# Performance work log

Measured on AMD Instinct MI355X. Metric: run time of the kernel, lower is better.

## Reference

```python
import jax, jax.numpy as jnp
import numpy as np


def conv(x, w, groups=1):
    # x: NCHW, w: OIHW, stride 1, SAME padding
    return jax.lax.conv_general_dilated(
        x, w, (1, 1), 'SAME', feature_group_count=groups,
        dimension_numbers=('NCHW', 'OIHW', 'NCHW'))


def bn(x, scale, shift):
    # eval-mode BatchNorm folded into per-channel affine
    return x * scale[None, :, None, None] + shift[None, :, None, None]


def ghost_expert(x, Wp, sp, bp, Wc, sc, bc, out_ch):
    # primary conv 3x3 (C_in -> init_ch) + BN + SiLU
    x1 = jax.nn.silu(bn(conv(x, Wp), sp, bp))
    # cheap depthwise 3x3 (groups = init_ch) + BN + SiLU
    x2 = jax.nn.silu(bn(conv(x1, Wc, groups=x1.shape[1]), sc, bc))
    return jnp.concatenate([x1, x2], axis=1)[:, :out_ch]


def setup_inputs() -> dict:
    key = jax.random.key(0)
    ks = jax.random.split(key, 20)
    B, Cin, Cout, H, W = 8, 256, 256, 64, 64
    E, red, init_ch, new_ch = 4, 32, 128, 128
    f = lambda k, shape, s=0.05: jax.random.normal(k, shape, jnp.float32) * s
    g = lambda k, shape: jax.random.uniform(k, shape, jnp.float32, 0.5, 1.5)
    inp = dict(
        x=jax.random.normal(ks[0], (B, Cin, H, W), jnp.float32),
        # router: conv3x3 Cin->red, BN, SiLU, conv1x1 red->E, BN
        Wr1=f(ks[1], (red, Cin, 3, 3)), sr1=g(ks[2], (red,)), br1=f(ks[3], (red,), 0.1),
        Wr2=f(ks[4], (E, red, 1, 1)), sr2=g(ks[5], (E,)), br2=f(ks[6], (E,), 0.1),
        # E ghost experts (stacked on leading expert axis)
        We_p=f(ks[7], (E, init_ch, Cin, 3, 3)), se_p=g(ks[8], (E, init_ch)), be_p=f(ks[9], (E, init_ch), 0.1),
        We_c=f(ks[10], (E, new_ch, 1, 3, 3)), se_c=g(ks[11], (E, new_ch)), be_c=f(ks[12], (E, new_ch), 0.1),
        # shared ghost expert
        Ws_p=f(ks[13], (init_ch, Cin, 3, 3)), ss_p=g(ks[14], (init_ch,)), bs_p=f(ks[15], (init_ch,), 0.1),
        Ws_c=f(ks[16], (new_ch, 1, 3, 3)), ss_c=g(ks[17], (new_ch,)), bs_c=f(ks[18], (new_ch,), 0.1),
        top_k=2,
    )
    return inp


def reference(x, Wr1, sr1, br1, Wr2, sr2, br2,
              We_p, se_p, be_p, We_c, se_c, be_c,
              Ws_p, ss_p, bs_p, Ws_c, ss_c, bs_c, top_k):
    B, Cin, H, W = x.shape
    E = Wr2.shape[0]
    Cout = 256
    pool_scale = 4
    # ---- EfficientSpatialRouter (eval mode: no noise) ----
    xd = x.reshape(B, Cin, H // pool_scale, pool_scale, W // pool_scale, pool_scale).mean((3, 5))
    h = jax.nn.silu(bn(conv(xd, Wr1), sr1, br1))
    logits = bn(conv(h, Wr2), sr2, br2)           # [B, E, H/4, W/4]
    global_logits = logits.mean(axis=(2, 3))      # [B, E]
    weights = jax.nn.softmax(global_logits, axis=1)
    topk_vals, topk_idx = jax.lax.top_k(weights, top_k)
    topk_vals = topk_vals / (topk_vals.sum(axis=1, keepdims=True) + 1e-6)
    # ---- dense all-expert compute + weighted combine ----
    run = lambda Wp, sp, bp, Wc, sc, bc: ghost_expert(x, Wp, sp, bp, Wc, sc, bc, Cout)
    expert_outs = jax.vmap(run)(We_p, se_p, be_p, We_c, se_c, be_c)  # [E,B,Cout,H,W]
    w_full = (topk_vals[:, :, None] * jax.nn.one_hot(topk_idx, E, dtype=x.dtype)).sum(1)  # [B,E]
    combined = jnp.einsum('be,ebchw->bchw', w_full, expert_outs)
    # ---- shared expert for stability ----
    shared = ghost_expert(x, Ws_p, ss_p, bs_p, Ws_c, ss_c, bs_c, Cout)
    return combined + shared
```

## Files before the change

kernel.cpp:

```cpp
#include <hip/hip_runtime.h>
#include <hip/hip_bf16.h>

constexpr int BATCH = 8;
constexpr int CIN   = 256;
constexpr int HH    = 64;
constexpr int WW    = 64;
constexpr int NPIX  = HH * WW;
constexpr int ICH   = 128;

constexpr size_t OFF_XD    = 0;
constexpr size_t OFF_HMEAN = 524288;
constexpr size_t OFF_WFULL = 524544;
constexpr size_t OFF_SLOT  = 524608;
constexpr size_t OFF_WTB   = 524672;
constexpr size_t OFF_XB    = OFF_WTB + 737280;
constexpr size_t OFF_X1B   = OFF_XB + 4194304;

typedef __bf16  bf16x8 __attribute__((ext_vector_type(8)));
typedef float   f32x4  __attribute__((ext_vector_type(4)));

__device__ __forceinline__ float silu_f(float v) { return v / (1.f + __expf(-v)); }

__device__ __forceinline__ unsigned short f2bf(float f) {
    return __builtin_bit_cast(unsigned short, __float2bfloat16(f));
}
__device__ __forceinline__ float bf2f(unsigned short u) {
    return __builtin_bit_cast(float, (unsigned)u << 16);
}
__device__ __forceinline__ bf16x8 ld_frag(const ushort* p) {
    uint4 v = *(const uint4*)p;
    return __builtin_bit_cast(bf16x8, v);
}

__global__ void k_avgpool(const float* __restrict__ x, float* __restrict__ xd)
{
    int t = blockIdx.x * 256 + threadIdx.x;
    int jb = t & 3, i = (t >> 2) & 15, c = (t >> 6) & 255, b = t >> 14;
    const float* src = x + ((size_t)(b * CIN + c) * HH + i * 4) * WW + jb * 16;
    float s0 = 0.f, s1 = 0.f, s2 = 0.f, s3 = 0.f;
#pragma unroll
    for (int r = 0; r < 4; ++r) {
        const float4* p = (const float4*)(src + r * WW);
        float4 a = p[0], b4 = p[1], c4 = p[2], d4 = p[3];
        s0 += a.x + a.y + a.z + a.w;
        s1 += b4.x + b4.y + b4.z + b4.w;
        s2 += c4.x + c4.y + c4.z + c4.w;
        s3 += d4.x + d4.y + d4.z + d4.w;
    }
    float4 o;
    o.x = s0 * 0.0625f; o.y = s1 * 0.0625f; o.z = s2 * 0.0625f; o.w = s3 * 0.0625f;
    *(float4*)(xd + ((size_t)(b * CIN + c) * 16 + i) * 16 + jb * 4) = o;
}

__global__ __launch_bounds__(256) void k_xprep(const float* __restrict__ x,
                                               ushort* __restrict__ xb)
{
    int b = blockIdx.x >> 6, row = blockIdx.x & 63;
    __shared__ ushort tile[64 * 258];
    int tid = threadIdx.x;
    const float* src = x + ((size_t)b * CIN * HH + row) * WW;
    for (int k = tid; k < 256 * 64; k += 256) {
        int cin = k >> 6, col = k & 63;
        tile[col * 258 + cin] = f2bf(src[(size_t)cin * NPIX + col]);
    }
    __syncthreads();
    ushort* dst = xb + (size_t)(b * 64 + row) * 64 * 256;
    for (int k = tid; k < 64 * 128; k += 256) {
        int col = k >> 7, cp = (k & 127) * 2;
        unsigned u0 = tile[col * 258 + cp];
        unsigned u1 = tile[col * 258 + cp + 1];
        *(unsigned*)(dst + (size_t)col * 256 + cp) = u0 | (u1 << 16);
    }
}

__global__ __launch_bounds__(256) void k_router_conv(
    const float* __restrict__ xd, const float* __restrict__ Wr1,
    const float* __restrict__ sr1, const float* __restrict__ br1,
    float* __restrict__ hmean)
{
    int b = blockIdx.x >> 5, r = blockIdx.x & 31;
    __shared__ float wl[9 * 256];
    __shared__ float red[256];
    int tid = threadIdx.x;
    for (int k = tid; k < 2304; k += 256) {
        int cin = k / 9, tap = k % 9;
        wl[tap * 256 + cin] = Wr1[r * 2304 + k];
    }
    __syncthreads();
    const float* xb = xd + (size_t)b * CIN * 256;
    int i = tid >> 4, j = tid & 15;
    float acc = 0.f;
#pragma unroll
    for (int kh = 0; kh < 3; ++kh) {
        int ii = i + kh - 1;
        bool oki = (unsigned)ii < 16u;
        int iis = oki ? ii : 0;
#pragma unroll
        for (int kw = 0; kw < 3; ++kw) {
            int jj = j + kw - 1;
            bool ok = oki && ((unsigned)jj < 16u);
            int off = iis * 16 + (((unsigned)jj < 16u) ? jj : 0);
            const float* wt = wl + (kh * 3 + kw) * 256;
            float t = 0.f;
#pragma unroll 8
            for (int cin = 0; cin < 256; ++cin)
                t = fmaf(wt[cin], xb[cin * 256 + off], t);
            if (ok) acc += t;
        }
    }
    float h = silu_f(acc * sr1[r] + br1[r]);
    red[tid] = h;
    __syncthreads();
    for (int st = 128; st > 0; st >>= 1) {
        if (tid < st) red[tid] += red[tid + st];
        __syncthreads();
    }
    if (tid == 0) hmean[b * 32 + r] = red[0] * (1.f / 256.f);
}

__global__ void k_router_final(const float* __restrict__ hmean,
                               const float* __restrict__ Wr2, const float* __restrict__ sr2,
                               const float* __restrict__ br2, const int* __restrict__ topk_p,
                               float* __restrict__ wfull, int* __restrict__ slot)
{
    __shared__ float lg[8][4];
    __shared__ float wf[8][5];
    int tid = threadIdx.x;
    if (tid < 32) {
        int b = tid >> 2, e = tid & 3;
        float a = 0.f;
        for (int r = 0; r < 32; ++r) a += Wr2[e * 32 + r] * hmean[b * 32 + r];
        lg[b][e] = a * sr2[e] + br2[e];
    }
    __syncthreads();
    if (tid < 8) {
        int b = tid;
        float l0 = lg[b][0], l1 = lg[b][1], l2 = lg[b][2], l3 = lg[b][3];
        float mx = fmaxf(fmaxf(l0, l1), fmaxf(l2, l3));
        float e0 = __expf(l0 - mx), e1 = __expf(l1 - mx), e2 = __expf(l2 - mx), e3 = __expf(l3 - mx);
        float sum = e0 + e1 + e2 + e3;
        float w[4] = { e0 / sum, e1 / sum, e2 / sum, e3 / sum };
        int k = topk_p[0];
        if (k > 4) k = 4;
        bool taken[4] = { false, false, false, false };
        float tv[4]; int ti[4]; float tsum = 0.f;
        for (int t = 0; t < k; ++t) {
            float best = -1e30f; int bi = 0;
            for (int e = 0; e < 4; ++e)
                if (!taken[e] && w[e] > best) { best = w[e]; bi = e; }
            taken[bi] = true; tv[t] = best; ti[t] = bi; tsum += best;
        }
        float inv = 1.f / (tsum + 1e-6f);
        float o[4] = { 0.f, 0.f, 0.f, 0.f };
        for (int t = 0; t < k; ++t) o[ti[t]] = tv[t] * inv;
        for (int e = 0; e < 4; ++e) { wf[b][e] = o[e]; wfull[b * 5 + e] = o[e]; }
        wf[b][4] = 1.f; wfull[b * 5 + 4] = 1.f;
    }
    __syncthreads();
    if (tid == 0) {
        int cnt = 0;
        for (int s = 0; s < 5; ++s)
            for (int b = 0; b < 8; ++b)
                slot[s * 8 + b] = (wf[b][s] != 0.f) ? (cnt++) : -1;
    }
}

__global__ void k_wprep16(const float* __restrict__ We_p, const float* __restrict__ Ws_p,
                          ushort* __restrict__ wtb)
{
    int t = blockIdx.x * 256 + threadIdx.x;
    int k5  = t & 31;
    int oc  = (t >> 5) & 63;
    int tap = (t >> 11) % 9;
    int blk = t / 18432;
    int chunk = blk & 7;
    int h     = (blk >> 3) & 1;
    int s     = blk >> 4;
    int cin   = chunk * 32 + k5;
    int ocg   = h * 64 + oc;
    float v = (s < 4) ? We_p[((size_t)(s * 128 + ocg) * 256 + cin) * 9 + tap]
                      : Ws_p[((size_t)ocg * 256 + cin) * 9 + tap];
    wtb[t] = f2bf(v);
}

__global__ __launch_bounds__(256, 2) void k_primary_mfma(
    const ushort* __restrict__ xb, const ushort* __restrict__ wtb,
    const float* __restrict__ se_p, const float* __restrict__ be_p,
    const float* __restrict__ ss_p, const float* __restrict__ bs_p,
    const int* __restrict__ slot, ushort* __restrict__ x1b)
{
    int pass = blockIdx.y;
    int sl = slot[pass];
    if (sl < 0) return;
    int s = pass >> 3, b = pass & 7;
    int och = blockIdx.x >> 4;
    int tile = blockIdx.x & 15;
    int row0 = (tile >> 2) * 16, col0 = (tile & 3) * 16;

    __shared__ ushort wlds[2304 * 8];
    __shared__ ushort xlds[1296 * 8];

    int tid = threadIdx.x;
    int w = tid >> 6, l = tid & 63;
    int ks = l >> 4, c = l & 15;

    f32x4 acc[4][4];
#pragma unroll
    for (int m = 0; m < 4; ++m)
#pragma unroll
        for (int n = 0; n < 4; ++n) acc[m][n] = (f32x4){0.f, 0.f, 0.f, 0.f};

    const ushort* wslab = wtb + (size_t)(s * 2 + och) * 8 * 18432;
    const ushort* xbase = xb + (size_t)b * 64 * 64 * 256;

    for (int ch = 0; ch < 8; ++ch) {
        __syncthreads();
        const ushort* wsrc = wslab + ch * 18432;
        for (int k = tid; k < 2304; k += 256) {
            uint4 v = *(const uint4*)(wsrc + k * 8);
            *(uint4*)(wlds + k * 8) = v;
        }
        int cin0 = ch * 32;
        for (int k = tid; k < 1296; k += 256) {
            int r = k / 72, rem = k % 72;
            int ks2 = rem / 18, c2 = rem % 18;
            int gr = row0 + r - 1, gc = col0 + c2 - 1;
            uint4 v = make_uint4(0u, 0u, 0u, 0u);
            if ((unsigned)gr < 64u && (unsigned)gc < 64u)
                v = *(const uint4*)(xbase + ((size_t)gr * 64 + gc) * 256 + cin0 + ks2 * 8);
            *(uint4*)(xlds + (size_t)k * 8) = v;
        }
        __syncthreads();
#pragma unroll
        for (int kh = 0; kh < 3; ++kh) {
#pragma unroll
            for (int kw = 0; kw < 3; ++kw) {
                int tap = kh * 3 + kw;
                bf16x8 afr[4];
#pragma unroll
                for (int m = 0; m < 4; ++m)
                    afr[m] = ld_frag(wlds + ((size_t)(tap * 64 + m * 16 + c) * 4 + ks) * 8);
#pragma unroll
                for (int n = 0; n < 4; ++n) {
                    int rloc = 4 * w + n + kh;
                    bf16x8 bfr = ld_frag(xlds + ((size_t)(rloc * 4 + ks) * 18 + c + kw) * 8);
#pragma unroll
                    for (int m = 0; m < 4; ++m)
                        acc[m][n] = __builtin_amdgcn_mfma_f32_16x16x32_bf16(
                            afr[m], bfr, acc[m][n], 0, 0, 0);
                }
            }
        }
    }

    const float* scale = (s < 4) ? (se_p + s * ICH) : ss_p;
    const float* shift = (s < 4) ? (be_p + s * ICH) : bs_p;
    ushort* outp = x1b + (size_t)sl * (ICH * NPIX);
    int colg = col0 + c;
#pragma unroll
    for (int m = 0; m < 4; ++m) {
#pragma unroll
        for (int n = 0; n < 4; ++n) {
            int rowg = row0 + 4 * w + n;
#pragma unroll
            for (int j = 0; j < 4; ++j) {
                int oc = och * 64 + m * 16 + ks * 4 + j;
                float v = acc[m][n][j] * scale[oc] + shift[oc];
                outp[(size_t)oc * NPIX + rowg * 64 + colg] = f2bf(silu_f(v));
            }
        }
    }
}

__global__ __launch_bounds__(256) void k_cheap(
    const ushort* __restrict__ x1b, const float* __restrict__ We_c,
    const float* __restrict__ se_c, const float* __restrict__ be_c,
    const float* __restrict__ Ws_c, const float* __restrict__ ss_c,
    const float* __restrict__ bs_c, const float* __restrict__ wfull,
    const int* __restrict__ slot, float* __restrict__ out)
{
    int blk = blockIdx.x;
    int b = blk >> 7, c = blk & 127;
    __shared__ float img[66][66];
    int tid = threadIdx.x;
    for (int k = tid; k < 66 * 66; k += 256) ((float*)img)[k] = 0.f;
    float o1[16], o2[16];
#pragma unroll
    for (int t = 0; t < 16; ++t) { o1[t] = 0.f; o2[t] = 0.f; }
    __syncthreads();

    for (int s = 0; s < 5; ++s) {
        int sl = slot[s * 8 + b];
        if (sl < 0) continue;
        float wgt = (s < 4) ? wfull[b * 5 + s] : 1.0f;
        const ushort* src = x1b + ((size_t)sl * ICH + c) * NPIX;
        for (int k = tid; k < NPIX / 2; k += 256) {
            int i = k >> 5, jc = (k & 31) * 2;
            unsigned u = *(const unsigned*)(src + i * 64 + jc);
            img[1 + i][1 + jc] = bf2f((unsigned short)(u & 0xFFFFu));
            img[1 + i][2 + jc] = bf2f((unsigned short)(u >> 16));
        }
        float wc[9], sc, sh;
        if (s < 4) {
            const float* wp = We_c + (size_t)(s * ICH + c) * 9;
#pragma unroll
            for (int t = 0; t < 9; ++t) wc[t] = wp[t];
            sc = se_c[s * ICH + c]; sh = be_c[s * ICH + c];
        } else {
            const float* wp = Ws_c + (size_t)c * 9;
#pragma unroll
            for (int t = 0; t < 9; ++t) wc[t] = wp[t];
            sc = ss_c[c]; sh = bs_c[c];
        }
        __syncthreads();
#pragma unroll
        for (int t = 0; t < 16; ++t) {
            int p = tid + t * 256;
            int i = p >> 6, j = p & 63;
            float center = img[1 + i][1 + j];
            float d = 0.f;
#pragma unroll
            for (int kh = 0; kh < 3; ++kh)
#pragma unroll
                for (int kw = 0; kw < 3; ++kw)
                    d = fmaf(wc[kh * 3 + kw], img[i + kh][j + kw], d);
            float v = d * sc + sh;
            o1[t] += wgt * center;
            o2[t] += wgt * silu_f(v);
        }
        __syncthreads();
    }

    float* out1 = out + ((size_t)(b * 256) + c) * NPIX;
    float* out2 = out + ((size_t)(b * 256) + 128 + c) * NPIX;
#pragma unroll
    for (int t = 0; t < 16; ++t) {
        int p = tid + t * 256;
        out1[p] = o1[t];
        out2[p] = o2[t];
    }
}

extern "C" void kernel_launch(void* const* d_in, const int* in_sizes, int n_in,
                              void* d_out, int out_size, void* d_ws, size_t ws_size,
                              hipStream_t stream)
{
    const float* x    = (const float*)d_in[0];
    const float* Wr1  = (const float*)d_in[1];
    const float* sr1  = (const float*)d_in[2];
    const float* br1  = (const float*)d_in[3];
    const float* Wr2  = (const float*)d_in[4];
    const float* sr2  = (const float*)d_in[5];
    const float* br2  = (const float*)d_in[6];
    const float* We_p = (const float*)d_in[7];
    const float* se_p = (const float*)d_in[8];
    const float* be_p = (const float*)d_in[9];
    const float* We_c = (const float*)d_in[10];
    const float* se_c = (const float*)d_in[11];
    const float* be_c = (const float*)d_in[12];
    const float* Ws_p = (const float*)d_in[13];
    const float* ss_p = (const float*)d_in[14];
    const float* bs_p = (const float*)d_in[15];
    const float* Ws_c = (const float*)d_in[16];
    const float* ss_c = (const float*)d_in[17];
    const float* bs_c = (const float*)d_in[18];
    const int*  topk  = (const int*)d_in[19];
    float* out = (float*)d_out;
    float* ws  = (float*)d_ws;

    float*  xd    = ws + OFF_XD;
    float*  hmean = ws + OFF_HMEAN;
    float*  wfull = ws + OFF_WFULL;
    int*    slot  = (int*)(ws + OFF_SLOT);
    ushort* wtb   = (ushort*)(ws + OFF_WTB);
    ushort* xb16  = (ushort*)(ws + OFF_XB);
    ushort* x1b   = (ushort*)(ws + OFF_X1B);

    k_avgpool<<<512, 256, 0, stream>>>(x, xd);
    k_xprep<<<512, 256, 0, stream>>>(x, xb16);
    k_wprep16<<<5760, 256, 0, stream>>>(We_p, Ws_p, wtb);
    k_router_conv<<<256, 256, 0, stream>>>(xd, Wr1, sr1, br1, hmean);
    k_router_final<<<1, 64, 0, stream>>>(hmean, Wr2, sr2, br2, topk, wfull, slot);
    k_primary_mfma<<<dim3(32, 40), 256, 0, stream>>>(xb16, wtb, se_p, be_p, ss_p, bs_p, slot, x1b);
    k_cheap<<<1024, 256, 0, stream>>>(x1b, We_c, se_c, be_c, Ws_c, ss_c, bs_c, wfull, slot, out);
}
```

Before: 315.4 us.

## Double-buffer input tiles via global_load_lds with zero-padded NHWC input

The input is stored in a zero-padded 66x66 NHWC bf16 buffer, cleared with a memset each call, so the conv tile load needs no bounds checks. Input tiles are fetched straight into a double-buffered LDS region with global_load_lds, and the next channel chunk is prefetched while MFMAs run on the current one. Weights are no longer staged in LDS: A fragments are read directly from global memory, which frees LDS so launch bounds rise to 3 blocks per CU. The risks are extra global and L2 traffic from the weight fragment reads, which are repeated across waves, and the cost of the memset.

```diff
diff --git a/kernel.cpp b/kernel.cpp
--- a/kernel.cpp
+++ b/kernel.cpp
@@ -13,8 +13,8 @@
 constexpr size_t OFF_WFULL = 524544;
 constexpr size_t OFF_SLOT  = 524608;
 constexpr size_t OFF_WTB   = 524672;
-constexpr size_t OFF_XB    = OFF_WTB + 737280;
-constexpr size_t OFF_X1B   = OFF_XB + 4194304;
+constexpr size_t OFF_XBP   = OFF_WTB + 737280;
+constexpr size_t OFF_X1B   = OFF_XBP + 4460544;
 
 typedef __bf16  bf16x8 __attribute__((ext_vector_type(8)));
 typedef float   f32x4  __attribute__((ext_vector_type(4)));
@@ -30,6 +30,11 @@
 __device__ __forceinline__ bf16x8 ld_frag(const ushort* p) {
     uint4 v = *(const uint4*)p;
     return __builtin_bit_cast(bf16x8, v);
+}
+__device__ __forceinline__ void gload16(const ushort* g, ushort* l) {
+    __builtin_amdgcn_global_load_lds(
+        (const __attribute__((address_space(1))) void*)g,
+        (__attribute__((address_space(3))) void*)l, 16, 0, 0);
 }
 
 __global__ void k_avgpool(const float* __restrict__ x, float* __restrict__ xd)
@@ -53,7 +58,7 @@
 }
 
 __global__ __launch_bounds__(256) void k_xprep(const float* __restrict__ x,
-                                               ushort* __restrict__ xb)
+                                               ushort* __restrict__ xbp)
 {
     int b = blockIdx.x >> 6, row = blockIdx.x & 63;
     __shared__ ushort tile[64 * 258];
@@ -64,7 +69,7 @@
         tile[col * 258 + cin] = f2bf(src[(size_t)cin * NPIX + col]);
     }
     __syncthreads();
-    ushort* dst = xb + (size_t)(b * 64 + row) * 64 * 256;
+    ushort* dst = xbp + ((size_t)(b * 66 + row + 1) * 66 + 1) * 256;
     for (int k = tid; k < 64 * 128; k += 256) {
         int col = k >> 7, cp = (k & 127) * 2;
         unsigned u0 = tile[col * 258 + cp];
@@ -183,8 +188,8 @@
     wtb[t] = f2bf(v);
 }
 
-__global__ __launch_bounds__(256, 2) void k_primary_mfma(
-    const ushort* __restrict__ xb, const ushort* __restrict__ wtb,
+__global__ __launch_bounds__(256, 3) void k_primary_mfma(
+    const ushort* __restrict__ xbp, const ushort* __restrict__ wtb,
     const float* __restrict__ se_p, const float* __restrict__ be_p,
     const float* __restrict__ ss_p, const float* __restrict__ bs_p,
     const int* __restrict__ slot, ushort* __restrict__ x1b)
@@ -197,12 +202,27 @@
     int tile = blockIdx.x & 15;
     int row0 = (tile >> 2) * 16, col0 = (tile & 3) * 16;
 
-    __shared__ ushort wlds[2304 * 8];
-    __shared__ ushort xlds[1296 * 8];
+    __shared__ ushort xlds[2][1344 * 8];
 
     int tid = threadIdx.x;
-    int w = tid >> 6, l = tid & 63;
-    int ks = l >> 4, c = l & 15;
+    int wv = tid >> 6, lane = tid & 63;
+    int ks = lane >> 4, c = lane & 15;
+
+    const ushort* xb_b = xbp + (size_t)b * 66 * 66 * 256;
+
+    int goff[6];
+#pragma unroll
+    for (int it = 0; it < 5; ++it) {
+        int k = it * 256 + tid;
+        int r = k / 72, rem = k % 72, ks2 = rem / 18, c2 = rem % 18;
+        goff[it] = ((row0 + r) * 66 + (col0 + c2)) * 256 + ks2 * 8;
+    }
+    {
+        int k = 1280 + lane;
+        int r = k / 72, rem = k % 72, ks2 = rem / 18, c2 = rem % 18;
+        goff[5] = ((row0 + r) * 66 + (col0 + c2)) * 256 + ks2 * 8;
+    }
+    int lds_us = wv * 512;
 
     f32x4 acc[4][4];
 #pragma unroll
@@ -210,27 +230,29 @@
 #pragma unroll
         for (int n = 0; n < 4; ++n) acc[m][n] = (f32x4){0.f, 0.f, 0.f, 0.f};
 
-    const ushort* wslab = wtb + (size_t)(s * 2 + och) * 8 * 18432;
-    const ushort* xbase = xb + (size_t)b * 64 * 64 * 256;
-
+    const ushort* wslab = wtb + (size_t)(s * 2 + och) * (8 * 18432);
+    int Sb = 4 * wv * 72 + ks * 18 + c;
+
+    {
+        const ushort* src = xb_b;
+#pragma unroll
+        for (int it = 0; it < 5; ++it)
+            gload16(src + goff[it], &xlds[0][(size_t)(it * 2048 + lds_us)]);
+        if (wv == 0) gload16(src + goff[5], &xlds[0][1280 * 8]);
+    }
+    __syncthreads();
+
+    int cur = 0;
     for (int ch = 0; ch < 8; ++ch) {
-        __syncthreads();
+        if (ch < 7) {
+            const ushort* src = xb_b + (ch + 1) * 32;
+#pragma unroll
+            for (int it = 0; it < 5; ++it)
+                gload16(src + goff[it], &xlds[cur ^ 1][(size_t)(it * 2048 + lds_us)]);
+            if (wv == 0) gload16(src + goff[5], &xlds[cur ^ 1][1280 * 8]);
+        }
         const ushort* wsrc = wslab + ch * 18432;
-        for (int k = tid; k < 2304; k += 256) {
-            uint4 v = *(const uint4*)(wsrc + k * 8);
-            *(uint4*)(wlds + k * 8) = v;
-        }
-        int cin0 = ch * 32;
-        for (int k = tid; k < 1296; k += 256) {
-            int r = k / 72, rem = k % 72;
-            int ks2 = rem / 18, c2 = rem % 18;
-            int gr = row0 + r - 1, gc = col0 + c2 - 1;
-            uint4 v = make_uint4(0u, 0u, 0u, 0u);
-            if ((unsigned)gr < 64u && (unsigned)gc < 64u)
-                v = *(const uint4*)(xbase + ((size_t)gr * 64 + gc) * 256 + cin0 + ks2 * 8);
-            *(uint4*)(xlds + (size_t)k * 8) = v;
-        }
-        __syncthreads();
+        const ushort* xl = &xlds[cur][0];
 #pragma unroll
         for (int kh = 0; kh < 3; ++kh) {
 #pragma unroll
@@ -239,11 +261,10 @@
                 bf16x8 afr[4];
 #pragma unroll
                 for (int m = 0; m < 4; ++m)
-                    afr[m] = ld_frag(wlds + ((size_t)(tap * 64 + m * 16 + c) * 4 + ks) * 8);
+                    afr[m] = ld_frag(wsrc + ((size_t)(tap * 64 + m * 16 + c) * 4 + ks) * 8);
 #pragma unroll
                 for (int n = 0; n < 4; ++n) {
-                    int rloc = 4 * w + n + kh;
-                    bf16x8 bfr = ld_frag(xlds + ((size_t)(rloc * 4 + ks) * 18 + c + kw) * 8);
+                    bf16x8 bfr = ld_frag(xl + (size_t)(Sb + (n + kh) * 72 + kw) * 8);
 #pragma unroll
                     for (int m = 0; m < 4; ++m)
                         acc[m][n] = __builtin_amdgcn_mfma_f32_16x16x32_bf16(
@@ -251,6 +272,8 @@
                 }
             }
         }
+        __syncthreads();
+        cur ^= 1;
     }
 
     const float* scale = (s < 4) ? (se_p + s * ICH) : ss_p;
@@ -261,7 +284,7 @@
     for (int m = 0; m < 4; ++m) {
 #pragma unroll
         for (int n = 0; n < 4; ++n) {
-            int rowg = row0 + 4 * w + n;
+            int rowg = row0 + 4 * wv + n;
 #pragma unroll
             for (int j = 0; j < 4; ++j) {
                 int oc = och * 64 + m * 16 + ks * 4 + j;
@@ -373,14 +396,15 @@
     float*  wfull = ws + OFF_WFULL;
     int*    slot  = (int*)(ws + OFF_SLOT);
     ushort* wtb   = (ushort*)(ws + OFF_WTB);
-    ushort* xb16  = (ushort*)(ws + OFF_XB);
+    ushort* xbp   = (ushort*)(ws + OFF_XBP);
     ushort* x1b   = (ushort*)(ws + OFF_X1B);
 
+    hipMemsetAsync(xbp, 0, (size_t)8 * 66 * 66 * 256 * sizeof(ushort), stream);
     k_avgpool<<<512, 256, 0, stream>>>(x, xd);
-    k_xprep<<<512, 256, 0, stream>>>(x, xb16);
+    k_xprep<<<512, 256, 0, stream>>>(x, xbp);
     k_wprep16<<<5760, 256, 0, stream>>>(We_p, Ws_p, wtb);
     k_router_conv<<<256, 256, 0, stream>>>(xd, Wr1, sr1, br1, hmean);
     k_router_final<<<1, 64, 0, stream>>>(hmean, Wr2, sr2, br2, topk, wfull, slot);
-    k_primary_mfma<<<dim3(32, 40), 256, 0, stream>>>(xb16, wtb, se_p, be_p, ss_p, bs_p, slot, x1b);
+    k_primary_mfma<<<dim3(32, 40), 256, 0, stream>>>(xbp, wtb, se_p, be_p, ss_p, bs_p, slot, x1b);
     k_cheap<<<1024, 256, 0, stream>>>(x1b, We_c, se_c, be_c, Ws_c, ss_c, bs_c, wfull, slot, out);
 }
```

New measurement: 365.0 us. +15.7%, slower.
